# Optimization experiments

Hardware: AMD Instinct MI355X
Metric: run time of the kernel (lower is better)

## Reference

```python
import jax, jax.numpy as jnp
import numpy as np

EPS_COMBINE = float(np.finfo(float).eps)  # combined[combined == 0] = np.finfo(float).eps
LOSS_COEF = 0.01


def cv_squared(v):
    # torch .var() is unbiased -> ddof=1
    return jnp.var(v, ddof=1) / (jnp.mean(v) ** 2 + 1e-10)


def setup_inputs() -> dict:
    key = jax.random.key(0)
    k1, k2, k3, k4 = jax.random.split(key, 4)
    B, D, E, C = 4096, 1024, 8, 4096
    x = jax.random.normal(k1, (B, D), jnp.float32)
    # small scale so exp(expert_out) in combine() stays finite
    w_gate = jax.random.normal(k2, (D, E), jnp.float32) * 0.02
    w_exp = jax.random.normal(k3, (E, D, C), jnp.float32) * 0.02
    b_exp = jax.random.normal(k4, (E, C), jnp.float32) * 0.02
    return {"x": x, "w_gate": w_gate, "w_exp": w_exp, "b_exp": b_exp, "k": 4}


def reference(x, w_gate, w_exp, b_exp, k):
    B, D = x.shape
    E = w_gate.shape[1]
    # --- noisy_top_k_gating with noisy_gating=False ---
    logits = x @ w_gate                                   # [B, E]
    top_logits, top_idx = jax.lax.top_k(logits, min(k + 1, E))
    topk_logits = top_logits[:, :k]
    topk_idx = top_idx[:, :k]
    topk_gates = jax.nn.softmax(topk_logits, axis=1)      # softmax over top-k only
    gates = jnp.zeros((B, E), x.dtype).at[jnp.arange(B)[:, None], topk_idx].set(topk_gates)
    importance = gates.sum(0)
    load = (gates > 0).sum(0).astype(jnp.float32)         # _gates_to_load
    loss = (cv_squared(importance) + cv_squared(load)) * LOSS_COEF
    # --- dispatch + per-expert forward + weighted combine ---
    # Experts with gate==0 contribute exactly 0 to the combine, so the dense
    # einsum over all experts computes the same math as SparseDispatcher.
    expert_out = jnp.einsum('bd,edc->bec', x, w_exp) + b_exp   # [B, E, C]
    combined = jnp.einsum('bec,be->bc', jnp.exp(expert_out), gates)  # weighted scatter-combine
    combined = jnp.where(combined == 0, EPS_COMBINE, combined)
    y = jnp.log(combined)
    return y, loss
```

## Files before the change

kernel.cpp:

```cpp
#include <hip/hip_runtime.h>
#include <stdint.h>

#define B_ROWS 4096
#define D_DIM  1024
#define E_NUM  8
#define C_DIM  4096
#define LOSS_COEF 0.01f
#define EPS_COMBINE 2.220446049250313e-16f

typedef float  f32x4  __attribute__((ext_vector_type(4)));
typedef __bf16 bf16x8 __attribute__((ext_vector_type(8)));

static __device__ __forceinline__ unsigned short f2bf(float f) {
    unsigned int u = __float_as_uint(f);
    u += 0x7fffu + ((u >> 16) & 1u);
    return (unsigned short)(u >> 16);
}

static __device__ __forceinline__ void async16(const void* g, void* l) {
    __builtin_amdgcn_global_load_lds(
        (const __attribute__((address_space(1))) unsigned int*)g,
        (__attribute__((address_space(3))) unsigned int*)l, 16, 0, 0);
}

__global__ void zero_stats_kernel(float* __restrict__ stats) {
    if (threadIdx.x < 16) stats[threadIdx.x] = 0.0f;
}

__global__ void cvt_x_kernel(const float4* __restrict__ xin, unsigned short* __restrict__ xb) {
    int i = blockIdx.x * blockDim.x + threadIdx.x;
    float4 v = xin[i];
    unsigned short h[4] = { f2bf(v.x), f2bf(v.y), f2bf(v.z), f2bf(v.w) };
    *(uint2*)(xb + (size_t)i * 4) = *(const uint2*)h;
}

__global__ __launch_bounds__(256) void transpose_wexp_kernel(
    const float* __restrict__ wexp, unsigned short* __restrict__ wT) {
    __shared__ float T[64][65];
    const int e  = blockIdx.z;
    const int k0 = blockIdx.y * 64;
    const int c0 = blockIdx.x * 64;
    const int t  = threadIdx.x;
    const int cc = t & 63;
    const int kb = t >> 6;
    const float* src = wexp + ((size_t)e * D_DIM + k0) * C_DIM + c0;
    #pragma unroll
    for (int i = 0; i < 16; ++i) {
        int kr = i * 4 + kb;
        T[kr][cc] = src[(size_t)kr * C_DIM + cc];
    }
    __syncthreads();
    #pragma unroll
    for (int j = 0; j < 2; ++j) {
        int chunk = j * 256 + t;
        int cl = chunk >> 3;
        int k8 = (chunk & 7) * 8;
        unsigned short h[8];
        #pragma unroll
        for (int i = 0; i < 8; ++i) h[i] = f2bf(T[k8 + i][cl]);
        *(uint4*)(wT + ((size_t)(e * C_DIM + c0 + cl)) * D_DIM + k0 + k8) =
            *(const uint4*)h;
    }
}

__global__ void gating_kernel(const float* __restrict__ x,
                              const float* __restrict__ wg,
                              float* __restrict__ gates,
                              float* __restrict__ stats) {
    __shared__ float simp[E_NUM], sload[E_NUM];
    const int tid = threadIdx.x;
    if (tid < E_NUM) { simp[tid] = 0.0f; sload[tid] = 0.0f; }
    __syncthreads();
    const int lane = tid & 63;
    const int wid  = tid >> 6;
    for (int i = 0; i < 16; ++i) {
        int row = blockIdx.x * 64 + wid * 16 + i;
        float acc[8] = {0.f,0.f,0.f,0.f,0.f,0.f,0.f,0.f};
        for (int d = lane; d < D_DIM; d += 64) {
            float xv = x[(size_t)row * D_DIM + d];
            const float4* wp = (const float4*)(wg + d * 8);
            float4 w0 = wp[0], w1 = wp[1];
            acc[0] += xv * w0.x; acc[1] += xv * w0.y;
            acc[2] += xv * w0.z; acc[3] += xv * w0.w;
            acc[4] += xv * w1.x; acc[5] += xv * w1.y;
            acc[6] += xv * w1.z; acc[7] += xv * w1.w;
        }
        #pragma unroll
        for (int off = 32; off > 0; off >>= 1)
            #pragma unroll
            for (int e = 0; e < 8; ++e)
                acc[e] += __shfl_xor(acc[e], off, 64);
        if (lane == 0) {
            float val[4]; int idx[4]; unsigned used = 0;
            #pragma unroll
            for (int j = 0; j < 4; ++j) {
                float best = -1e30f; int bi = 0;
                for (int ee = 0; ee < 8; ++ee)
                    if (!(used & (1u << ee)) && acc[ee] > best) { best = acc[ee]; bi = ee; }
                used |= 1u << bi; val[j] = best; idx[j] = bi;
            }
            float mx = val[0], sum = 0.f, gv[4];
            #pragma unroll
            for (int j = 0; j < 4; ++j) { gv[j] = __expf(val[j] - mx); sum += gv[j]; }
            float inv = 1.0f / sum;
            float gout[8] = {0.f,0.f,0.f,0.f,0.f,0.f,0.f,0.f};
            #pragma unroll
            for (int j = 0; j < 4; ++j) gout[idx[j]] = gv[j] * inv;
            #pragma unroll
            for (int e = 0; e < 8; ++e) gates[(size_t)row * 8 + e] = gout[e];
            #pragma unroll
            for (int j = 0; j < 4; ++j) {
                atomicAdd(&simp[idx[j]], gv[j] * inv);
                atomicAdd(&sload[idx[j]], 1.0f);
            }
        }
    }
    __syncthreads();
    if (tid < E_NUM) {
        atomicAdd(&stats[tid],          simp[tid]);
        atomicAdd(&stats[E_NUM + tid],  sload[tid]);
    }
}

__global__ void loss_kernel(const float* __restrict__ stats, float* __restrict__ out_loss) {
    if (threadIdx.x == 0) {
        float mi = 0.f, ml = 0.f;
        for (int e = 0; e < 8; ++e) { mi += stats[e]; ml += stats[8 + e]; }
        mi *= 0.125f; ml *= 0.125f;
        float vi = 0.f, vl = 0.f;
        for (int e = 0; e < 8; ++e) {
            float a = stats[e] - mi;     vi += a * a;
            float b = stats[8 + e] - ml; vl += b * b;
        }
        vi *= (1.0f / 7.0f); vl *= (1.0f / 7.0f);
        out_loss[0] = (vi / (mi * mi + 1e-10f) + vl / (ml * ml + 1e-10f)) * LOSS_COEF;
    }
}

__global__ __launch_bounds__(256, 3) void moe_main_kernel(
    const unsigned short* __restrict__ xb,
    const unsigned short* __restrict__ wT,
    const float* __restrict__ bexp,
    const float* __restrict__ gates,
    float* __restrict__ out)
{
    __shared__ unsigned short As[128 * 32];
    __shared__ unsigned short Bs[128 * 32];
    __shared__ float gs[128 * 8];
    __shared__ float bs[8 * 128];

    const int tid  = threadIdx.x;
    const int lane = tid & 63;
    const int wid  = tid >> 6;
    const int wm   = wid >> 1;
    const int wn   = wid & 1;
    const int q    = lane >> 4;
    const int ln   = lane & 15;
    const int row0 = blockIdx.x * 128;
    const int col0 = blockIdx.y * 128;

    ((float4*)gs)[tid] = ((const float4*)(gates + (size_t)row0 * 8))[tid];
    {
        int e = tid >> 5, c4 = (tid & 31) * 4;
        *(float4*)(bs + e * 128 + c4) = *(const float4*)(bexp + (size_t)e * C_DIM + col0 + c4);
    }

    const f32x4 vzero = {0.f, 0.f, 0.f, 0.f};
    f32x4 comb[4][4];
    #pragma unroll
    for (int i = 0; i < 4; ++i)
        #pragma unroll
        for (int j = 0; j < 4; ++j) comb[i][j] = vzero;

    const int rS = tid >> 2;
    const int qg = (tid & 3) ^ (rS & 3);
    const unsigned short* gA = xb + (size_t)(row0 + rS) * D_DIM + qg * 8;
    const unsigned short* gBb = wT + ((size_t)(col0 + rS)) * D_DIM + qg * 8;
    char* ldsA = (char*)As + wid * 1024;
    char* ldsB = (char*)Bs + wid * 1024;

    const int fq = (q << 3) ^ ((ln & 3) << 3);

    for (int e = 0; e < E_NUM; ++e) {
        f32x4 acc[4][4];
        #pragma unroll
        for (int i = 0; i < 4; ++i)
            #pragma unroll
            for (int j = 0; j < 4; ++j) acc[i][j] = vzero;

        const unsigned short* gB = gBb + (size_t)e * C_DIM * D_DIM;

        for (int kt = 0; kt < D_DIM / 32; ++kt) {
            const unsigned short* ga = gA + kt * 32;
            const unsigned short* gb = gB + kt * 32;
            async16(ga,                ldsA);
            async16(ga + 64 * D_DIM,   ldsA + 4096);
            async16(gb,                ldsB);
            async16(gb + 64 * D_DIM,   ldsB + 4096);

            __syncthreads();

            bf16x8 af[4], bfr[4];
            #pragma unroll
            for (int fm = 0; fm < 4; ++fm)
                af[fm] = *(const bf16x8*)(As + (wm * 64 + fm * 16 + ln) * 32 + fq);
            #pragma unroll
            for (int fn = 0; fn < 4; ++fn)
                bfr[fn] = *(const bf16x8*)(Bs + (wn * 64 + fn * 16 + ln) * 32 + fq);
            #pragma unroll
            for (int fm = 0; fm < 4; ++fm)
                #pragma unroll
                for (int fn = 0; fn < 4; ++fn)
                    acc[fm][fn] = __builtin_amdgcn_mfma_f32_16x16x32_bf16(
                        af[fm], bfr[fn], acc[fm][fn], 0, 0, 0);

            __syncthreads();
        }

        #pragma unroll
        for (int fn = 0; fn < 4; ++fn) {
            float bval = bs[e * 128 + wn * 64 + fn * 16 + ln];
            #pragma unroll
            for (int fm = 0; fm < 4; ++fm)
                #pragma unroll
                for (int r = 0; r < 4; ++r) {
                    float g = gs[(wm * 64 + fm * 16 + q * 4 + r) * 8 + e];
                    comb[fm][fn][r] += g * __expf(acc[fm][fn][r] + bval);
                }
        }
    }

    #pragma unroll
    for (int fm = 0; fm < 4; ++fm)
        #pragma unroll
        for (int fn = 0; fn < 4; ++fn)
            #pragma unroll
            for (int r = 0; r < 4; ++r) {
                int row = row0 + wm * 64 + fm * 16 + q * 4 + r;
                int col = col0 + wn * 64 + fn * 16 + ln;
                float c = comb[fm][fn][r];
                c = (c == 0.0f) ? EPS_COMBINE : c;
                out[(size_t)row * C_DIM + col] = __logf(c);
            }
}

extern "C" void kernel_launch(void* const* d_in, const int* in_sizes, int n_in,
                              void* d_out, int out_size, void* d_ws, size_t ws_size,
                              hipStream_t stream) {
    const float* x    = (const float*)d_in[0];
    const float* wg   = (const float*)d_in[1];
    const float* wexp = (const float*)d_in[2];
    const float* bexp = (const float*)d_in[3];
    float* out = (float*)d_out;
    char*  ws  = (char*)d_ws;

    unsigned short* wT    = (unsigned short*)ws;
    unsigned short* xb    = (unsigned short*)(ws + 67108864);
    float*          gates = (float*)(ws + 75497472);
    float*          stats = (float*)(ws + 75628544);

    zero_stats_kernel<<<1, 64, 0, stream>>>(stats);
    {
        dim3 tg(C_DIM / 64, D_DIM / 64, E_NUM);
        transpose_wexp_kernel<<<tg, 256, 0, stream>>>(wexp, wT);
    }
    cvt_x_kernel<<<(B_ROWS * D_DIM / 4) / 256, 256, 0, stream>>>((const float4*)x, xb);
    gating_kernel<<<B_ROWS / 64, 256, 0, stream>>>(x, wg, gates, stats);
    loss_kernel<<<1, 64, 0, stream>>>(stats, out + (size_t)B_ROWS * C_DIM);

    dim3 grid(B_ROWS / 128, C_DIM / 128);
    moe_main_kernel<<<grid, 256, 0, stream>>>(xb, wT, bexp, gates, out);
}
```

Before: 677.9 us.

## Fuse x conversion into gating, vectorize transpose, use 512-thread main GEMM blocks

The bf16 conversion of x moves into the gating kernel, which now handles one row per wave across more blocks, removing a separate kernel launch and a second read of x. The weight transpose loads float4 and writes 32-byte chunks per thread. The main MoE kernel switches to 512 threads with 8 waves in a 2x4 layout, halving per-wave accumulators to raise occupancy, and pads the gates LDS array to avoid bank conflicts. More waves per block add sync overhead, and each wave now does a smaller MFMA tile with less fragment reuse.

```diff
diff --git a/kernel.cpp b/kernel.cpp
--- a/kernel.cpp
+++ b/kernel.cpp
@@ -27,92 +27,91 @@
     if (threadIdx.x < 16) stats[threadIdx.x] = 0.0f;
 }
 
-__global__ void cvt_x_kernel(const float4* __restrict__ xin, unsigned short* __restrict__ xb) {
-    int i = blockIdx.x * blockDim.x + threadIdx.x;
-    float4 v = xin[i];
-    unsigned short h[4] = { f2bf(v.x), f2bf(v.y), f2bf(v.z), f2bf(v.w) };
-    *(uint2*)(xb + (size_t)i * 4) = *(const uint2*)h;
-}
-
 __global__ __launch_bounds__(256) void transpose_wexp_kernel(
     const float* __restrict__ wexp, unsigned short* __restrict__ wT) {
-    __shared__ float T[64][65];
+    __shared__ float T[64][68];
     const int e  = blockIdx.z;
     const int k0 = blockIdx.y * 64;
     const int c0 = blockIdx.x * 64;
     const int t  = threadIdx.x;
-    const int cc = t & 63;
-    const int kb = t >> 6;
     const float* src = wexp + ((size_t)e * D_DIM + k0) * C_DIM + c0;
     #pragma unroll
-    for (int i = 0; i < 16; ++i) {
-        int kr = i * 4 + kb;
-        T[kr][cc] = src[(size_t)kr * C_DIM + cc];
+    for (int i = 0; i < 4; ++i) {
+        int kr = i * 16 + (t >> 4);
+        int cg = (t & 15) * 4;
+        float4 v = *(const float4*)(src + (size_t)kr * C_DIM + cg);
+        *(float4*)&T[kr][cg] = v;
     }
     __syncthreads();
-    #pragma unroll
-    for (int j = 0; j < 2; ++j) {
-        int chunk = j * 256 + t;
-        int cl = chunk >> 3;
-        int k8 = (chunk & 7) * 8;
-        unsigned short h[8];
-        #pragma unroll
-        for (int i = 0; i < 8; ++i) h[i] = f2bf(T[k8 + i][cl]);
-        *(uint4*)(wT + ((size_t)(e * C_DIM + c0 + cl)) * D_DIM + k0 + k8) =
-            *(const uint4*)h;
-    }
-}
-
-__global__ void gating_kernel(const float* __restrict__ x,
-                              const float* __restrict__ wg,
-                              float* __restrict__ gates,
-                              float* __restrict__ stats) {
+    const int cl  = t & 63;
+    const int k16 = (t >> 6) * 16;
+    unsigned short h[16];
+    #pragma unroll
+    for (int j = 0; j < 16; ++j) h[j] = f2bf(T[k16 + j][cl]);
+    unsigned short* dst = wT + ((size_t)(e * C_DIM + c0 + cl)) * D_DIM + k0 + k16;
+    *(uint4*)dst       = ((const uint4*)h)[0];
+    *(uint4*)(dst + 8) = ((const uint4*)h)[1];
+}
+
+__global__ __launch_bounds__(256) void gating_kernel(
+    const float* __restrict__ x,
+    const float* __restrict__ wg,
+    unsigned short* __restrict__ xb,
+    float* __restrict__ gates,
+    float* __restrict__ stats) {
     __shared__ float simp[E_NUM], sload[E_NUM];
     const int tid = threadIdx.x;
     if (tid < E_NUM) { simp[tid] = 0.0f; sload[tid] = 0.0f; }
     __syncthreads();
     const int lane = tid & 63;
     const int wid  = tid >> 6;
-    for (int i = 0; i < 16; ++i) {
-        int row = blockIdx.x * 64 + wid * 16 + i;
-        float acc[8] = {0.f,0.f,0.f,0.f,0.f,0.f,0.f,0.f};
-        for (int d = lane; d < D_DIM; d += 64) {
-            float xv = x[(size_t)row * D_DIM + d];
-            const float4* wp = (const float4*)(wg + d * 8);
+    const int row  = blockIdx.x * 4 + wid;
+
+    float acc[8] = {0.f,0.f,0.f,0.f,0.f,0.f,0.f,0.f};
+    #pragma unroll
+    for (int i = 0; i < 4; ++i) {
+        int d = i * 256 + lane * 4;
+        float4 xv = *(const float4*)(x + (size_t)row * D_DIM + d);
+        unsigned short hh[4] = { f2bf(xv.x), f2bf(xv.y), f2bf(xv.z), f2bf(xv.w) };
+        *(uint2*)(xb + (size_t)row * D_DIM + d) = *(const uint2*)hh;
+        float xa[4] = { xv.x, xv.y, xv.z, xv.w };
+        #pragma unroll
+        for (int j = 0; j < 4; ++j) {
+            const float4* wp = (const float4*)(wg + (size_t)(d + j) * 8);
             float4 w0 = wp[0], w1 = wp[1];
-            acc[0] += xv * w0.x; acc[1] += xv * w0.y;
-            acc[2] += xv * w0.z; acc[3] += xv * w0.w;
-            acc[4] += xv * w1.x; acc[5] += xv * w1.y;
-            acc[6] += xv * w1.z; acc[7] += xv * w1.w;
-        }
-        #pragma unroll
-        for (int off = 32; off > 0; off >>= 1)
-            #pragma unroll
-            for (int e = 0; e < 8; ++e)
-                acc[e] += __shfl_xor(acc[e], off, 64);
-        if (lane == 0) {
-            float val[4]; int idx[4]; unsigned used = 0;
-            #pragma unroll
-            for (int j = 0; j < 4; ++j) {
-                float best = -1e30f; int bi = 0;
-                for (int ee = 0; ee < 8; ++ee)
-                    if (!(used & (1u << ee)) && acc[ee] > best) { best = acc[ee]; bi = ee; }
-                used |= 1u << bi; val[j] = best; idx[j] = bi;
-            }
-            float mx = val[0], sum = 0.f, gv[4];
-            #pragma unroll
-            for (int j = 0; j < 4; ++j) { gv[j] = __expf(val[j] - mx); sum += gv[j]; }
-            float inv = 1.0f / sum;
-            float gout[8] = {0.f,0.f,0.f,0.f,0.f,0.f,0.f,0.f};
-            #pragma unroll
-            for (int j = 0; j < 4; ++j) gout[idx[j]] = gv[j] * inv;
-            #pragma unroll
-            for (int e = 0; e < 8; ++e) gates[(size_t)row * 8 + e] = gout[e];
-            #pragma unroll
-            for (int j = 0; j < 4; ++j) {
-                atomicAdd(&simp[idx[j]], gv[j] * inv);
-                atomicAdd(&sload[idx[j]], 1.0f);
-            }
+            acc[0] += xa[j] * w0.x; acc[1] += xa[j] * w0.y;
+            acc[2] += xa[j] * w0.z; acc[3] += xa[j] * w0.w;
+            acc[4] += xa[j] * w1.x; acc[5] += xa[j] * w1.y;
+            acc[6] += xa[j] * w1.z; acc[7] += xa[j] * w1.w;
+        }
+    }
+    #pragma unroll
+    for (int off = 32; off > 0; off >>= 1)
+        #pragma unroll
+        for (int e = 0; e < 8; ++e)
+            acc[e] += __shfl_xor(acc[e], off, 64);
+    if (lane == 0) {
+        float val[4]; int idx[4]; unsigned used = 0;
+        #pragma unroll
+        for (int j = 0; j < 4; ++j) {
+            float best = -1e30f; int bi = 0;
+            for (int ee = 0; ee < 8; ++ee)
+                if (!(used & (1u << ee)) && acc[ee] > best) { best = acc[ee]; bi = ee; }
+            used |= 1u << bi; val[j] = best; idx[j] = bi;
+        }
+        float mx = val[0], sum = 0.f, gv[4];
+        #pragma unroll
+        for (int j = 0; j < 4; ++j) { gv[j] = __expf(val[j] - mx); sum += gv[j]; }
+        float inv = 1.0f / sum;
+        float gout[8] = {0.f,0.f,0.f,0.f,0.f,0.f,0.f,0.f};
+        #pragma unroll
+        for (int j = 0; j < 4; ++j) gout[idx[j]] = gv[j] * inv;
+        #pragma unroll
+        for (int e = 0; e < 8; ++e) gates[(size_t)row * 8 + e] = gout[e];
+        #pragma unroll
+        for (int j = 0; j < 4; ++j) {
+            atomicAdd(&simp[idx[j]], gv[j] * inv);
+            atomicAdd(&sload[idx[j]], 1.0f);
         }
     }
     __syncthreads();
@@ -137,7 +136,7 @@
     }
 }
 
-__global__ __launch_bounds__(256, 3) void moe_main_kernel(
+__global__ __launch_bounds__(512, 4) void moe_main_kernel(
     const unsigned short* __restrict__ xb,
     const unsigned short* __restrict__ wT,
     const float* __restrict__ bexp,
@@ -146,71 +145,68 @@
 {
     __shared__ unsigned short As[128 * 32];
     __shared__ unsigned short Bs[128 * 32];
-    __shared__ float gs[128 * 8];
+    __shared__ float gs[128 * 9];
     __shared__ float bs[8 * 128];
 
     const int tid  = threadIdx.x;
     const int lane = tid & 63;
     const int wid  = tid >> 6;
-    const int wm   = wid >> 1;
-    const int wn   = wid & 1;
+    const int wm   = wid >> 2;
+    const int wn   = wid & 3;
     const int q    = lane >> 4;
     const int ln   = lane & 15;
     const int row0 = blockIdx.x * 128;
     const int col0 = blockIdx.y * 128;
 
-    ((float4*)gs)[tid] = ((const float4*)(gates + (size_t)row0 * 8))[tid];
+    for (int i = tid; i < 1024; i += 512)
+        gs[(i >> 3) * 9 + (i & 7)] = gates[(size_t)row0 * 8 + i];
     {
-        int e = tid >> 5, c4 = (tid & 31) * 4;
-        *(float4*)(bs + e * 128 + c4) = *(const float4*)(bexp + (size_t)e * C_DIM + col0 + c4);
+        int e = tid >> 6, c2 = (tid & 63) * 2;
+        *(float2*)(bs + e * 128 + c2) = *(const float2*)(bexp + (size_t)e * C_DIM + col0 + c2);
     }
 
     const f32x4 vzero = {0.f, 0.f, 0.f, 0.f};
-    f32x4 comb[4][4];
+    f32x4 comb[4][2];
     #pragma unroll
     for (int i = 0; i < 4; ++i)
         #pragma unroll
-        for (int j = 0; j < 4; ++j) comb[i][j] = vzero;
+        for (int j = 0; j < 2; ++j) comb[i][j] = vzero;
 
     const int rS = tid >> 2;
     const int qg = (tid & 3) ^ (rS & 3);
-    const unsigned short* gA = xb + (size_t)(row0 + rS) * D_DIM + qg * 8;
-    const unsigned short* gBb = wT + ((size_t)(col0 + rS)) * D_DIM + qg * 8;
+    const unsigned short* gA  = xb + (size_t)(row0 + rS) * D_DIM + qg * 8;
+    const unsigned short* gBb = wT + (size_t)(col0 + rS) * D_DIM + qg * 8;
     char* ldsA = (char*)As + wid * 1024;
     char* ldsB = (char*)Bs + wid * 1024;
 
-    const int fq = (q << 3) ^ ((ln & 3) << 3);
+    const int fq = ((q ^ (ln & 3)) << 3);
 
     for (int e = 0; e < E_NUM; ++e) {
-        f32x4 acc[4][4];
+        f32x4 acc[4][2];
         #pragma unroll
         for (int i = 0; i < 4; ++i)
             #pragma unroll
-            for (int j = 0; j < 4; ++j) acc[i][j] = vzero;
+            for (int j = 0; j < 2; ++j) acc[i][j] = vzero;
 
         const unsigned short* gB = gBb + (size_t)e * C_DIM * D_DIM;
 
         for (int kt = 0; kt < D_DIM / 32; ++kt) {
-            const unsigned short* ga = gA + kt * 32;
-            const unsigned short* gb = gB + kt * 32;
-            async16(ga,                ldsA);
-            async16(ga + 64 * D_DIM,   ldsA + 4096);
-            async16(gb,                ldsB);
-            async16(gb + 64 * D_DIM,   ldsB + 4096);
+            async16(gA + kt * 32, ldsA);
+            async16(gB + kt * 32, ldsB);
 
             __syncthreads();
 
-            bf16x8 af[4], bfr[4];
+            bf16x8 af[4], bfr[2];
             #pragma unroll
             for (int fm = 0; fm < 4; ++fm)
                 af[fm] = *(const bf16x8*)(As + (wm * 64 + fm * 16 + ln) * 32 + fq);
             #pragma unroll
-            for (int fn = 0; fn < 4; ++fn)
-                bfr[fn] = *(const bf16x8*)(Bs + (wn * 64 + fn * 16 + ln) * 32 + fq);
+            for (int fn = 0; fn < 2; ++fn)
+                bfr[fn] = *(const bf16x8*)(Bs + (wn * 32 + fn * 16 + ln) * 32 + fq);
             #pragma unroll
             for (int fm = 0; fm < 4; ++fm)
                 #pragma unroll
-                for (int fn = 0; fn < 4; ++fn)
+                for (int fn = 0; fn < 2; ++fn)
                     acc[fm][fn] = __builtin_amdgcn_mfma_f32_16x16x32_bf16(
                         af[fm], bfr[fn], acc[fm][fn], 0, 0, 0);
 
@@ -218,13 +214,13 @@
         }
 
         #pragma unroll
-        for (int fn = 0; fn < 4; ++fn) {
-            float bval = bs[e * 128 + wn * 64 + fn * 16 + ln];
+        for (int fn = 0; fn < 2; ++fn) {
+            float bval = bs[e * 128 + wn * 32 + fn * 16 + ln];
             #pragma unroll
             for (int fm = 0; fm < 4; ++fm)
                 #pragma unroll
                 for (int r = 0; r < 4; ++r) {
-                    float g = gs[(wm * 64 + fm * 16 + q * 4 + r) * 8 + e];
+                    float g = gs[(wm * 64 + fm * 16 + q * 4 + r) * 9 + e];
                     comb[fm][fn][r] += g * __expf(acc[fm][fn][r] + bval);
                 }
         }
@@ -233,11 +229,11 @@
     #pragma unroll
     for (int fm = 0; fm < 4; ++fm)
         #pragma unroll
-        for (int fn = 0; fn < 4; ++fn)
+        for (int fn = 0; fn < 2; ++fn)
             #pragma unroll
             for (int r = 0; r < 4; ++r) {
                 int row = row0 + wm * 64 + fm * 16 + q * 4 + r;
-                int col = col0 + wn * 64 + fn * 16 + ln;
+                int col = col0 + wn * 32 + fn * 16 + ln;
                 float c = comb[fm][fn][r];
                 c = (c == 0.0f) ? EPS_COMBINE : c;
                 out[(size_t)row * C_DIM + col] = __logf(c);
@@ -264,10 +260,9 @@
         dim3 tg(C_DIM / 64, D_DIM / 64, E_NUM);
         transpose_wexp_kernel<<<tg, 256, 0, stream>>>(wexp, wT);
     }
-    cvt_x_kernel<<<(B_ROWS * D_DIM / 4) / 256, 256, 0, stream>>>((const float4*)x, xb);
-    gating_kernel<<<B_ROWS / 64, 256, 0, stream>>>(x, wg, gates, stats);
+    gating_kernel<<<B_ROWS / 4, 256, 0, stream>>>(x, wg, xb, gates, stats);
     loss_kernel<<<1, 64, 0, stream>>>(stats, out + (size_t)B_ROWS * C_DIM);
 
     dim3 grid(B_ROWS / 128, C_DIM / 128);
-    moe_main_kernel<<<grid, 256, 0, stream>>>(xb, wT, bexp, gates, out);
-}
+    moe_main_kernel<<<grid, 512, 0, stream>>>(xb, wT, bexp, gates, out);
+}
```

Measured after the change: 612.8 us. 1.11x faster.
